# Kernel optimization log

Measured on AMD Instinct MI355X. Metric: run time of the kernel, lower is better.

## Reference

```python
import jax, jax.numpy as jnp
import numpy as np

N_NODES = 100000
N_EDGES = 3200000
B = 64            # number of graphs / RNA batch
DIM = 16          # GINE hidden dim
NFP = 33          # protein node feature dim
EMB = 128         # embedding dim
MAXLEN = 3000     # rna_global length (conv1d in_channels)
LOCLEN = 2998     # rna_local length = 3000 - log4(64) + 1
NF = 32           # n_filters
KS = 8            # conv kernel size -> 128-8+1 = 121
FC_IN = NF * 121  # 3872
BN_EPS = 1e-5


def setup_inputs() -> dict:
    key = jax.random.key(0)
    ks = jax.random.split(key, 32)
    s = 0.1
    p = {}
    # forward data args
    p['pro_x'] = jax.random.normal(ks[0], (N_NODES, NFP), jnp.float32)
    p['pro_edge_index'] = jax.random.randint(ks[1], (2, N_EDGES), 0, N_NODES, jnp.int32)
    p['pro_weight'] = jax.random.uniform(ks[2], (N_EDGES, 1), jnp.float32)
    p['pro_batch'] = jnp.sort(jax.random.randint(ks[3], (N_NODES,), 0, B, jnp.int32))
    p['rna_global'] = jax.random.randint(ks[4], (B, MAXLEN), 0, 5, jnp.int32)
    p['rna_local'] = jax.random.randint(ks[5], (B, LOCLEN), 0, 65, jnp.int32)
    # GINE layer 1 (33 -> 16)
    p['g1_w1'] = jax.random.normal(ks[6], (NFP, DIM), jnp.float32) * s
    p['g1_b1'] = jnp.zeros((DIM,), jnp.float32)
    p['g1_w2'] = jax.random.normal(ks[7], (DIM, DIM), jnp.float32) * s
    p['g1_b2'] = jnp.zeros((DIM,), jnp.float32)
    p['g1_ew'] = jax.random.normal(ks[8], (1, NFP), jnp.float32) * s  # edge Linear(1, 33)
    p['g1_eb'] = jnp.zeros((NFP,), jnp.float32)
    p['g1_eps'] = jnp.zeros((), jnp.float32)
    # GINE layers 2-5 (16 -> 16), stacked on leading axis
    p['g_w1'] = jax.random.normal(ks[9], (4, DIM, DIM), jnp.float32) * s
    p['g_b1'] = jnp.zeros((4, DIM), jnp.float32)
    p['g_w2'] = jax.random.normal(ks[10], (4, DIM, DIM), jnp.float32) * s
    p['g_b2'] = jnp.zeros((4, DIM), jnp.float32)
    p['g_ew'] = jax.random.normal(ks[11], (4, 1, DIM), jnp.float32) * s  # edge Linear(1, 16)
    p['g_eb'] = jnp.zeros((4, DIM), jnp.float32)
    p['g_eps'] = jnp.zeros((4,), jnp.float32)
    # BatchNorm1d x5
    p['bn_gamma'] = jnp.ones((5, DIM), jnp.float32)
    p['bn_beta'] = jnp.zeros((5, DIM), jnp.float32)
    # fc1_xp (16 -> 128)
    p['fc1_xp_w'] = jax.random.normal(ks[12], (DIM, EMB), jnp.float32) * s
    p['fc1_xp_b'] = jnp.zeros((EMB,), jnp.float32)
    # RNA branch
    p['emb1'] = jax.random.normal(ks[13], (5, EMB), jnp.float32)
    p['emb2'] = jax.random.normal(ks[14], (65, EMB), jnp.float32)
    p['convr1_w'] = jax.random.normal(ks[15], (NF, MAXLEN, KS), jnp.float32) * 0.01
    p['convr1_b'] = jnp.zeros((NF,), jnp.float32)
    p['convr2_w'] = jax.random.normal(ks[16], (NF, LOCLEN, KS), jnp.float32) * 0.01
    p['convr2_b'] = jnp.zeros((NF,), jnp.float32)
    p['fcxr_w'] = jax.random.normal(ks[17], (FC_IN, EMB), jnp.float32) * 0.01
    p['fcxr_b'] = jnp.zeros((EMB,), jnp.float32)
    return p


def _gine(x, src, dst, ew, w1, b1, w2, b2, ew_w, ew_b, eps):
    # GINEConv: out = MLP((1+eps)*x + sum_j relu(x_j + edge_lin(e_ij)))
    e = ew @ ew_w + ew_b                       # [E, d]
    m = jax.nn.relu(x[src] + e)                # [E, d] gather + fuse
    agg = jax.ops.segment_sum(m, dst, num_segments=N_NODES)
    h = (1.0 + eps) * x + agg
    return jax.nn.relu(h @ w1 + b1) @ w2 + b2


def _bn(x, gamma, beta):
    mu = jnp.mean(x, axis=0)
    var = jnp.var(x, axis=0)
    return (x - mu) * jax.lax.rsqrt(var + BN_EPS) * gamma + beta


def _rna_branch(tokens, emb, cw, cb, fcw, fcb):
    x = emb[tokens]                            # [B, L, 128]
    y = jax.lax.conv_general_dilated(x, cw, (1,), 'VALID',
                                     dimension_numbers=('NCH', 'OIH', 'NCH'))
    y = y + cb[None, :, None]                  # [B, 32, 121]
    return y.reshape(y.shape[0], -1) @ fcw + fcb


def reference(pro_x, pro_edge_index, pro_weight, pro_batch, rna_global, rna_local,
              g1_w1, g1_b1, g1_w2, g1_b2, g1_ew, g1_eb, g1_eps,
              g_w1, g_b1, g_w2, g_b2, g_ew, g_eb, g_eps,
              bn_gamma, bn_beta, fc1_xp_w, fc1_xp_b,
              emb1, emb2, convr1_w, convr1_b, convr2_w, convr2_b, fcxr_w, fcxr_b):
    src, dst = pro_edge_index[0], pro_edge_index[1]
    # RNA global / local branches (shared fc_xr)
    xrg = _rna_branch(rna_global, emb1, convr1_w, convr1_b, fcxr_w, fcxr_b)
    xrl = _rna_branch(rna_local, emb2, convr2_w, convr2_b, fcxr_w, fcxr_b)
    # protein GINE stack
    xp = jax.nn.relu(_gine(pro_x, src, dst, pro_weight,
                           g1_w1, g1_b1, g1_w2, g1_b2, g1_ew, g1_eb, g1_eps))
    xp = _bn(xp, bn_gamma[0], bn_beta[0])
    for i in range(4):
        xp = jax.nn.relu(_gine(xp, src, dst, pro_weight,
                               g_w1[i], g_b1[i], g_w2[i], g_b2[i],
                               g_ew[i], g_eb[i], g_eps[i]))
        xp = _bn(xp, bn_gamma[i + 1], bn_beta[i + 1])
    # global mean pool over graphs
    sums = jax.ops.segment_sum(xp, pro_batch, num_segments=B)
    cnt = jax.ops.segment_sum(jnp.ones((N_NODES, 1), xp.dtype), pro_batch, num_segments=B)
    xp = jax.nn.relu((sums / jnp.maximum(cnt, 1.0)) @ fc1_xp_w + fc1_xp_b)
    # dropout in eval mode -> identity
    xc_rna = 0.5 * (xrg + xrl)
    return (xc_rna, xp)
```

## Files before the change

kernel.cpp:

```cpp
#include <hip/hip_runtime.h>
#include <hip/hip_fp16.h>

#define N_NODES 100000
#define N_EDGES 3200000
#define BGR 64
#define DIM 16
#define NFP 33
#define ROW1 32
#define H1STR 36
#define EMB 128
#define MAXLEN 3000
#define LOCLEN 2998
#define NF 32
#define KS 8
#define OUTT 121
#define FC_IN 3872
#define BN_EPSV 1e-5f
#define POOL_CHUNK 256
#define POOL_BLKS 391
#define MLPB 391
#define AGGB1 6250
#define AGGB16 3125
#define NBIN 391
#define BCNT_BLK 512
#define P1_CHUNK 4096
#define P1_BLOCKS 782
#define MAXBIN 9088
#define NKC 32
#define KCH 121
#define WDEC (1.f / 32767.f)
#define SEG_G 8

__global__ void __launch_bounds__(256) k_bincnt(const int* __restrict__ dst,
                                                int* __restrict__ bh) {
    __shared__ int hist[NBIN];
    int t = threadIdx.x, bid = blockIdx.x;
    for (int b = t; b < NBIN; b += 256) hist[b] = 0;
    __syncthreads();
    int e0 = bid * (N_EDGES / BCNT_BLK);
    int e1 = e0 + (N_EDGES / BCNT_BLK);
    for (int e = e0 + t; e < e1; e += 256) atomicAdd(&hist[dst[e] >> 8], 1);
    __syncthreads();
    for (int b = t; b < NBIN; b += 256) bh[b * BCNT_BLK + bid] = hist[b];
}

__global__ void __launch_bounds__(512) k_binscan(const int* __restrict__ bh,
                                                 int* __restrict__ binoff,
                                                 int* __restrict__ bincur) {
    __shared__ int sc[512];
    int t = threadIdx.x;
    int s = 0;
    if (t < NBIN) {
        const int4* row = (const int4*)(bh + t * BCNT_BLK);
        #pragma unroll 4
        for (int k = 0; k < BCNT_BLK / 4; k++) {
            int4 v = row[k];
            s += v.x + v.y + v.z + v.w;
        }
    }
    sc[t] = s;
    __syncthreads();
    for (int off = 1; off < 512; off <<= 1) {
        int v = (t >= off) ? sc[t - off] : 0;
        __syncthreads();
        sc[t] += v;
        __syncthreads();
    }
    int excl = sc[t] - s;
    if (t <= NBIN) binoff[t] = excl;
    if (t < NBIN) bincur[t] = excl;
}

__global__ void __launch_bounds__(256) k_part1(const int* __restrict__ src,
                                               const int* __restrict__ dst,
                                               const float* __restrict__ w,
                                               int* __restrict__ bincur,
                                               int2* __restrict__ tmp_sw) {
    __shared__ int2 srec[P1_CHUNK];
    __shared__ unsigned short sbin[P1_CHUNK];
    __shared__ unsigned short sperm[P1_CHUNK];
    __shared__ int hist[NBIN];
    __shared__ int off[NBIN];
    __shared__ int cur[NBIN];
    __shared__ int base[NBIN];
    __shared__ int sc[512];
    int t = threadIdx.x;
    int g0 = blockIdx.x * P1_CHUNK;
    int cn = N_EDGES - g0; if (cn > P1_CHUNK) cn = P1_CHUNK;
    for (int b = t; b < NBIN; b += 256) hist[b] = 0;
    __syncthreads();
    for (int j = t; j < cn; j += 256) {
        int d = dst[g0 + j];
        int b = d >> 8;
        sbin[j] = (unsigned short)b;
        srec[j] = make_int2(src[g0 + j] | ((d & 255) << 20), __float_as_int(w[g0 + j]));
        atomicAdd(&hist[b], 1);
    }
    __syncthreads();
    sc[t] = (t < NBIN) ? hist[t] : 0;
    sc[256 + t] = (256 + t < NBIN) ? hist[256 + t] : 0;
    __syncthreads();
    for (int o = 1; o <= 256; o <<= 1) {
        int v0 = (t >= o) ? sc[t - o] : 0;
        int v1 = sc[256 + t - o];
        __syncthreads();
        sc[t] += v0;
        sc[256 + t] += v1;
        __syncthreads();
    }
    for (int b = t; b < NBIN; b += 256) {
        int e = sc[b] - hist[b];
        off[b] = e;
        cur[b] = e;
        int c = hist[b];
        base[b] = c ? atomicAdd(&bincur[b], c) : 0;
    }
    __syncthreads();
    for (int j = t; j < cn; j += 256) {
        int p = atomicAdd(&cur[sbin[j]], 1);
        sperm[p] = (unsigned short)j;
    }
    __syncthreads();
    for (int p = t; p < cn; p += 256) {
        int j = sperm[p];
        int b = sbin[j];
        tmp_sw[base[b] + (p - off[b])] = srec[j];
    }
}

__global__ void __launch_bounds__(256) k_part2(const int2* __restrict__ tmp_sw,
                                               const int* __restrict__ binoff,
                                               unsigned* __restrict__ er,
                                               int* __restrict__ ptr) {
    __shared__ unsigned char sdl[MAXBIN];
    __shared__ unsigned short perm[MAXBIN];
    __shared__ int hist[256];
    __shared__ int cur[256];
    __shared__ int sc[256];
    int t = threadIdx.x, b = blockIdx.x;
    int nlo = b << 8;
    int e0 = binoff[b], e1 = binoff[b + 1];
    int cnt = e1 - e0;
    int stage = cnt < MAXBIN ? cnt : MAXBIN;
    hist[t] = 0;
    __syncthreads();
    for (int j = t; j < stage; j += 256) {
        unsigned char dl = (unsigned char)((tmp_sw[e0 + j].x >> 20) & 255);
        sdl[j] = dl;
        atomicAdd(&hist[dl], 1);
    }
    for (int j = stage + t; j < cnt; j += 256)
        atomicAdd(&hist[(tmp_sw[e0 + j].x >> 20) & 255], 1);
    __syncthreads();
    int v = hist[t];
    sc[t] = v;
    __syncthreads();
    for (int off = 1; off < 256; off <<= 1) {
        int u = (t >= off) ? sc[t - off] : 0;
        __syncthreads();
        sc[t] += u;
        __syncthreads();
    }
    int excl = sc[t] - v;
    cur[t] = excl;
    if (nlo + t < N_NODES) ptr[nlo + t] = e0 + excl;
    if (b == NBIN - 1 && t == 0) ptr[N_NODES] = N_EDGES;
    __syncthreads();
    for (int j = t; j < stage; j += 256) {
        int p = atomicAdd(&cur[sdl[j]], 1);
        perm[p] = (unsigned short)j;
    }
    __syncthreads();
    for (int j = stage + t; j < cnt; j += 256) {
        int2 sw = tmp_sw[e0 + j];
        int p = atomicAdd(&cur[(sw.x >> 20) & 255], 1);
        unsigned wq = (unsigned)(__int_as_float(sw.y) * 32767.f + 0.5f);
        er[e0 + p] = ((unsigned)sw.x & 0x1FFFFu) | (wq << 17);
    }
    for (int p = t; p < stage; p += 256) {
        int2 sw = tmp_sw[e0 + perm[p]];
        unsigned wq = (unsigned)(__int_as_float(sw.y) * 32767.f + 0.5f);
        er[e0 + p] = ((unsigned)sw.x & 0x1FFFFu) | (wq << 17);
    }
}

__global__ void k_half1(const float* __restrict__ x, __half* __restrict__ xh,
                        __half* __restrict__ xh32) {
    int i = blockIdx.x * blockDim.x + threadIdx.x;
    if (i < N_NODES * NFP) {
        int n = i / NFP, f = i - n * NFP;
        __half v = __float2half(x[i]);
        if (f < 32) xh[n * ROW1 + f] = v;
        else xh32[n] = v;
    }
}

__global__ void __launch_bounds__(256) k_cwt2(const float* __restrict__ cw1,
                                              const float* __restrict__ cw2,
                                              float* __restrict__ cwTg,
                                              float* __restrict__ cwTl) {
    int l = blockIdx.x;
    int ok = threadIdx.x;
    if (l < MAXLEN) {
        cwTg[l * 256 + ok] = cw1[(ok >> 3) * (MAXLEN * KS) + l * KS + (ok & 7)];
    } else {
        int ll = l - MAXLEN;
        cwTl[ll * 256 + ok] = cw2[(ok >> 3) * (LOCLEN * KS) + ll * KS + (ok & 7)];
    }
}

__device__ __forceinline__ void acc8p(float a[8], uint4 r, float wv,
                                      const float* __restrict__ ewf,
                                      const float* __restrict__ ebf) {
    float2 f01 = __half22float2(*(__half2*)&r.x);
    float2 f23 = __half22float2(*(__half2*)&r.y);
    float2 f45 = __half22float2(*(__half2*)&r.z);
    float2 f67 = __half22float2(*(__half2*)&r.w);
    float x[8] = {f01.x, f01.y, f23.x, f23.y, f45.x, f45.y, f67.x, f67.y};
    #pragma unroll
    for (int j = 0; j < 8; j++)
        a[j] += fmaxf(x[j] + fmaf(wv, ewf[j], ebf[j]), 0.f);
}

__device__ __forceinline__ void acc8s(float a[8], uint4 r, float wv,
                                      const float* __restrict__ scf,
                                      const float* __restrict__ cbf,
                                      const float* __restrict__ ewf) {
    float2 f01 = __half22float2(*(__half2*)&r.x);
    float2 f23 = __half22float2(*(__half2*)&r.y);
    float2 f45 = __half22float2(*(__half2*)&r.z);
    float2 f67 = __half22float2(*(__half2*)&r.w);
    float x[8] = {f01.x, f01.y, f23.x, f23.y, f45.x, f45.y, f67.x, f67.y};
    #pragma unroll
    for (int j = 0; j < 8; j++)
        a[j] += fmaxf(fmaf(x[j], scf[j], fmaf(wv, ewf[j], cbf[j])), 0.f);
}

__global__ void __launch_bounds__(256) k_agg1(
    const __half* __restrict__ xh, const __half* __restrict__ xh32,
    const int* __restrict__ ptr, const unsigned* __restrict__ er,
    const float* __restrict__ ew, const float* __restrict__ ebv,
    const float* __restrict__ epsp, float* __restrict__ h) {
    int t = threadIdx.x;
    int wave = t >> 6, lane = t & 63;
    int nl = lane >> 4;
    int slot = (lane >> 2) & 3;
    int q = lane & 3;
    float ewf[8], ebf[8];
    #pragma unroll
    for (int j = 0; j < 8; j++) { ewf[j] = ew[q * 8 + j]; ebf[j] = ebv[q * 8 + j]; }
    float ew32 = ew[32], eb32 = ebv[32];
    float ep = 1.f + epsp[0];
    int node = blockIdx.x * 16 + wave * 4 + nl;
    int e0 = ptr[node], e1 = ptr[node + 1];
    float a[8] = {0, 0, 0, 0, 0, 0, 0, 0};
    float a32 = 0.f;
    int i = e0 + slot;
    while (i + 4 < e1) {
        unsigned ev0 = er[i];
        unsigned ev1 = er[i + 4];
        int s0 = ev0 & 0x1FFFF, s1 = ev1 & 0x1FFFF;
        float wv0 = (float)(ev0 >> 17) * WDEC;
        float wv1 = (float)(ev1 >> 17) * WDEC;
        uint4 r0 = *(const uint4*)(xh + s0 * ROW1 + q * 8);
        uint4 r1 = *(const uint4*)(xh + s1 * ROW1 + q * 8);
        acc8p(a, r0, wv0, ewf, ebf);
        acc8p(a, r1, wv1, ewf, ebf);
        if (q == 0) {
            a32 += fmaxf(__half2float(xh32[s0]) + fmaf(wv0, ew32, eb32), 0.f);
            a32 += fmaxf(__half2float(xh32[s1]) + fmaf(wv1, ew32, eb32), 0.f);
        }
        i += 8;
    }
    if (i < e1) {
        unsigned ev = er[i];
        int s = ev & 0x1FFFF;
        float wv = (float)(ev >> 17) * WDEC;
        uint4 r = *(const uint4*)(xh + s * ROW1 + q * 8);
        acc8p(a, r, wv, ewf, ebf);
        if (q == 0)
            a32 += fmaxf(__half2float(xh32[s]) + fmaf(wv, ew32, eb32), 0.f);
    }
    #pragma unroll
    for (int j = 0; j < 8; j++) {
        a[j] += __shfl_xor(a[j], 4);
        a[j] += __shfl_xor(a[j], 8);
    }
    a32 += __shfl_xor(a32, 4);
    a32 += __shfl_xor(a32, 8);
    if (slot == 0) {
        uint4 sraw = *(const uint4*)(xh + node * ROW1 + q * 8);
        float2 s01 = __half22float2(*(__half2*)&sraw.x);
        float2 s23 = __half22float2(*(__half2*)&sraw.y);
        float2 s45 = __half22float2(*(__half2*)&sraw.z);
        float2 s67 = __half22float2(*(__half2*)&sraw.w);
        float* hp = h + node * H1STR + q * 8;
        *(float4*)hp = make_float4(ep * s01.x + a[0], ep * s01.y + a[1],
                                   ep * s23.x + a[2], ep * s23.y + a[3]);
        *(float4*)(hp + 4) = make_float4(ep * s45.x + a[4], ep * s45.y + a[5],
                                         ep * s67.x + a[6], ep * s67.y + a[7]);
        if (q == 0)
            h[node * H1STR + 32] = ep * __half2float(xh32[node]) + a32;
    }
}

__global__ void __launch_bounds__(256) k_agg16(
    const __half* __restrict__ zh, const int* __restrict__ ptr,
    const unsigned* __restrict__ er,
    const float* __restrict__ ew, const float* __restrict__ ebv,
    const float* __restrict__ epsp,
    const float* __restrict__ bnstat, const float* __restrict__ gamma,
    const float* __restrict__ beta, float* __restrict__ h) {
    int t = threadIdx.x;
    int wave = t >> 6, lane = t & 63;
    int nl = lane >> 3;
    int slot = (lane >> 1) & 3;
    int hh = lane & 1;
    float ep = 1.f + epsp[0];
    const float invn = 1.f / (float)N_NODES;
    float scf[8], shf[8], cbf[8], ewf[8];
    #pragma unroll
    for (int j = 0; j < 8; j++) {
        int f = hh * 8 + j;
        float mu = bnstat[f] * invn;
        float var = bnstat[DIM + f] * invn - mu * mu;
        float sc = gamma[f] * rsqrtf(var + BN_EPSV);
        scf[j] = sc;
        shf[j] = beta[f] - mu * sc;
        cbf[j] = shf[j] + ebv[f];
        ewf[j] = ew[f];
    }
    int node = blockIdx.x * 32 + wave * 8 + nl;
    int e0 = ptr[node], e1 = ptr[node + 1];
    float a[8] = {0, 0, 0, 0, 0, 0, 0, 0};
    int i = e0 + slot;
    while (i + 4 < e1) {
        unsigned ev0 = er[i];
        unsigned ev1 = er[i + 4];
        float wv0 = (float)(ev0 >> 17) * WDEC;
        float wv1 = (float)(ev1 >> 17) * WDEC;
        uint4 r0 = *(const uint4*)(zh + (ev0 & 0x1FFFFu) * DIM + hh * 8);
        uint4 r1 = *(const uint4*)(zh + (ev1 & 0x1FFFFu) * DIM + hh * 8);
        acc8s(a, r0, wv0, scf, cbf, ewf);
        acc8s(a, r1, wv1, scf, cbf, ewf);
        i += 8;
    }
    if (i < e1) {
        unsigned ev = er[i];
        float wv = (float)(ev >> 17) * WDEC;
        uint4 r = *(const uint4*)(zh + (ev & 0x1FFFFu) * DIM + hh * 8);
        acc8s(a, r, wv, scf, cbf, ewf);
    }
    #pragma unroll
    for (int j = 0; j < 8; j++) a[j] += __shfl_xor(a[j], 2);
    #pragma unroll
    for (int j = 0; j < 8; j++) a[j] += __shfl_xor(a[j], 4);
    if (slot == 0) {
        uint4 sraw = *(const uint4*)(zh + node * DIM + hh * 8);
        float2 s01 = __half22float2(*(__half2*)&sraw.x);
        float2 s23 = __half22float2(*(__half2*)&sraw.y);
        float2 s45 = __half22float2(*(__half2*)&sraw.z);
        float2 s67 = __half22float2(*(__half2*)&sraw.w);
        float xs[8] = {s01.x, s01.y, s23.x, s23.y, s45.x, s45.y, s67.x, s67.y};
        float o8[8];
        #pragma unroll
        for (int j = 0; j < 8; j++)
            o8[j] = ep * fmaf(xs[j], scf[j], shf[j]) + a[j];
        float* hp = h + node * DIM + hh * 8;
        *(float4*)hp = make_float4(o8[0], o8[1], o8[2], o8[3]);
        *(float4*)(hp + 4) = make_float4(o8[4], o8[5], o8[6], o8[7]);
    }
}

__device__ __forceinline__ void mlp_bn_tail(float zv[16], bool active, int t,
                                            float* __restrict__ bnstat) {
    __shared__ float red[4][32];
    float zs[16], zq[16];
    #pragma unroll
    for (int o = 0; o < 16; o++) {
        zs[o] = active ? zv[o] : 0.f;
        zq[o] = active ? zv[o] * zv[o] : 0.f;
    }
    #pragma unroll
    for (int m = 1; m <= 32; m <<= 1) {
        #pragma unroll
        for (int o = 0; o < 16; o++) {
            zs[o] += __shfl_xor(zs[o], m);
            zq[o] += __shfl_xor(zq[o], m);
        }
    }
    int wave = t >> 6, lane = t & 63;
    if (lane == 0) {
        #pragma unroll
        for (int o = 0; o < 16; o++) {
            red[wave][o] = zs[o];
            red[wave][16 + o] = zq[o];
        }
    }
    __syncthreads();
    if (t < 32)
        atomicAdd(&bnstat[t], red[0][t] + red[1][t] + red[2][t] + red[3][t]);
}

__device__ __forceinline__ void store_zh(__half* __restrict__ zh, int n, float zv[16]) {
    __half2 p[8];
    #pragma unroll
    for (int j = 0; j < 8; j++) p[j] = __floats2half2_rn(zv[2 * j], zv[2 * j + 1]);
    *(uint4*)(zh + n * DIM) = *(uint4*)&p[0];
    *(uint4*)(zh + n * DIM + 8) = *(uint4*)&p[4];
}

__global__ void __launch_bounds__(256) k_mlp16(
    const float* __restrict__ h,
    const float* __restrict__ W1, const float* __restrict__ b1,
    const float* __restrict__ W2, const float* __restrict__ b2,
    __half* __restrict__ zh, float* __restrict__ bnstat) {
    __shared__ float W1s[256], W2s[256], b1s[16], b2s[16];
    int t = threadIdx.x;
    W1s[t] = W1[t];
    W2s[t] = W2[t];
    if (t < 16) { b1s[t] = b1[t]; b2s[t] = b2[t]; }
    __syncthreads();
    int n = blockIdx.x * 256 + t;
    bool active = n < N_NODES;
    float zv[16];
    if (active) {
        float hv[16];
        #pragma unroll
        for (int j = 0; j < 4; j++) {
            float4 v = *(const float4*)(h + n * DIM + j * 4);
            hv[j * 4] = v.x; hv[j * 4 + 1] = v.y; hv[j * 4 + 2] = v.z; hv[j * 4 + 3] = v.w;
        }
        float tv[16];
        #pragma unroll
        for (int o = 0; o < 16; o++) {
            float s = b1s[o];
            #pragma unroll
            for (int f = 0; f < 16; f++) s += hv[f] * W1s[f * 16 + o];
            tv[o] = fmaxf(s, 0.f);
        }
        #pragma unroll
        for (int o = 0; o < 16; o++) {
            float s = b2s[o];
            #pragma unroll
            for (int f = 0; f < 16; f++) s += tv[f] * W2s[f * 16 + o];
            zv[o] = fmaxf(s, 0.f);
        }
        store_zh(zh, n, zv);
    }
    mlp_bn_tail(zv, active, t, bnstat);
}

__global__ void __launch_bounds__(256) k_mlp1(
    const float* __restrict__ h,
    const float* __restrict__ W1, const float* __restrict__ b1,
    const float* __restrict__ W2, const float* __restrict__ b2,
    __half* __restrict__ zh, float* __restrict__ bnstat) {
    __shared__ float W1s[NFP * 16], W2s[256], b1s[16], b2s[16];
    int t = threadIdx.x;
    for (int j = t; j < NFP * 16; j += 256) W1s[j] = W1[j];
    W2s[t] = W2[t];
    if (t < 16) { b1s[t] = b1[t]; b2s[t] = b2[t]; }
    __syncthreads();
    int n = blockIdx.x * 256 + t;
    bool active = n < N_NODES;
    float zv[16];
    if (active) {
        float hv[NFP];
        #pragma unroll
        for (int j = 0; j < 8; j++) {
            float4 v = *(const float4*)(h + n * H1STR + j * 4);
            hv[j * 4] = v.x; hv[j * 4 + 1] = v.y; hv[j * 4 + 2] = v.z; hv[j * 4 + 3] = v.w;
        }
        hv[32] = h[n * H1STR + 32];
        float tv[16];
        #pragma unroll
        for (int o = 0; o < 16; o++) {
            float s = b1s[o];
            #pragma unroll
            for (int f = 0; f < NFP; f++) s += hv[f] * W1s[f * 16 + o];
            tv[o] = fmaxf(s, 0.f);
        }
        #pragma unroll
        for (int o = 0; o < 16; o++) {
            float s = b2s[o];
            #pragma unroll
            for (int f = 0; f < 16; f++) s += tv[f] * W2s[f * 16 + o];
            zv[o] = fmaxf(s, 0.f);
        }
        store_zh(zh, n, zv);
    }
    mlp_bn_tail(zv, active, t, bnstat);
}

__global__ void __launch_bounds__(256) k_pool(const __half* __restrict__ zh,
                                              const int* __restrict__ batch,
                                              const float* __restrict__ bnstat,
                                              const float* __restrict__ gamma,
                                              const float* __restrict__ beta,
                                              float* __restrict__ gsum,
                                              float* __restrict__ gcnt) {
    __shared__ float lsum[BGR * DIM];
    __shared__ float lcnt[BGR];
    int t = threadIdx.x;
    for (int j = t; j < BGR * DIM; j += 256) lsum[j] = 0.f;
    if (t < BGR) lcnt[t] = 0.f;
    __syncthreads();
    int f = t & 15, r = t >> 4;
    const float invn = 1.f / (float)N_NODES;
    float mu = bnstat[f] * invn;
    float var = bnstat[DIM + f] * invn - mu * mu;
    float sc = gamma[f] * rsqrtf(var + BN_EPSV);
    float sh = beta[f] - mu * sc;
    int start = blockIdx.x * POOL_CHUNK;
    float acc = 0.f, cacc = 0.f;
    int cur = -1;
    for (int i = 0; i < POOL_CHUNK / 16; i++) {
        int n = start + r + i * 16;
        if (n >= N_NODES) break;
        int b = batch[n];
        if (b != cur) {
            if (cur >= 0) {
                atomicAdd(&lsum[cur * DIM + f], acc);
                if (f == 0) atomicAdd(&lcnt[cur], cacc);
            }
            cur = b; acc = 0.f; cacc = 0.f;
        }
        acc += fmaf(__half2float(zh[n * DIM + f]), sc, sh);
        cacc += 1.f;
    }
    if (cur >= 0) {
        atomicAdd(&lsum[cur * DIM + f], acc);
        if (f == 0) atomicAdd(&lcnt[cur], cacc);
    }
    __syncthreads();
    for (int j = t; j < BGR * DIM; j += 256) {
        float v = lsum[j];
        if (v != 0.f) atomicAdd(&gsum[j], v);
    }
    if (t < BGR) {
        float v = lcnt[t];
        if (v != 0.f) atomicAdd(&gcnt[t], v);
    }
}

__global__ void k_xp(const float* __restrict__ gsum, const float* __restrict__ gcnt,
                     const float* __restrict__ w, const float* __restrict__ bias,
                     float* __restrict__ out) {
    int b = blockIdx.x;
    int e = threadIdx.x;
    float inv = 1.f / fmaxf(gcnt[b], 1.f);
    float acc = bias[e];
    #pragma unroll
    for (int f = 0; f < DIM; f++) acc += gsum[b * DIM + f] * inv * w[f * EMB + e];
    out[b * EMB + e] = fmaxf(acc, 0.f);
}

__global__ void __launch_bounds__(256) k_bucket2(const int* __restrict__ tg,
                                                 const int* __restrict__ tl,
                                                 int* __restrict__ blg, int* __restrict__ bpg,
                                                 int* __restrict__ bll, int* __restrict__ bpl) {
    __shared__ int hist[65];
    __shared__ int cursor[65];
    int which = blockIdx.y;
    const int* tok = which ? tl : tg;
    int L = which ? LOCLEN : MAXLEN;
    int V = which ? 65 : 5;
    int* blist = which ? bll : blg;
    int* bptr = which ? bpl : bpg;
    int b = blockIdx.x, t = threadIdx.x;
    if (t < V) hist[t] = 0;
    __syncthreads();
    for (int l = t; l < L; l += 256) atomicAdd(&hist[tok[b * L + l]], 1);
    __syncthreads();
    if (t == 0) {
        int run = 0;
        for (int v = 0; v < V; v++) {
            cursor[v] = run;
            bptr[b * (V + 1) + v] = run;
            run += hist[v];
        }
        bptr[b * (V + 1) + V] = run;
    }
    __syncthreads();
    for (int l = t; l < L; l += 256) {
        int v = tok[b * L + l];
        int p = atomicAdd(&cursor[v], 1);
        blist[b * L + p] = l;
    }
}

__global__ void __launch_bounds__(256) k_wsum(const int* __restrict__ blg,
                                              const int* __restrict__ bpg,
                                              const int* __restrict__ bll,
                                              const int* __restrict__ bpl,
                                              const float* __restrict__ cwTg,
                                              const float* __restrict__ cwTl,
                                              float* __restrict__ Wp,
                                              float* __restrict__ Wlocal) {
    int b = blockIdx.x, y = blockIdx.y;
    int t = threadIdx.x;
    if (y < 40) {
        int v = y >> 3, seg = y & 7;
        int s = bpg[b * 6 + v], e = bpg[b * 6 + v + 1];
        int cnt = e - s;
        int chunk = (cnt + SEG_G - 1) / SEG_G;
        int j0 = s + seg * chunk;
        int j1 = j0 + chunk; if (j1 > e) j1 = e;
        const int* bl = blg + b * MAXLEN;
        float acc = 0.f;
        int j = j0;
        while (j + 3 < j1) {
            int t0 = bl[j], t1 = bl[j + 1], t2 = bl[j + 2], t3 = bl[j + 3];
            float a0 = cwTg[t0 * 256 + t];
            float a1 = cwTg[t1 * 256 + t];
            float a2 = cwTg[t2 * 256 + t];
            float a3 = cwTg[t3 * 256 + t];
            acc += a0 + a1 + a2 + a3;
            j += 4;
        }
        while (j < j1) {
            acc += cwTg[bl[j] * 256 + t];
            j++;
        }
        Wp[((b * 5 + v) * SEG_G + seg) * 256 + t] = acc;
    } else {
        int v = y - 40;
        int s = bpl[b * 66 + v], e = bpl[b * 66 + v + 1];
        const int* bl = bll + b * LOCLEN;
        float acc = 0.f;
        int j = s;
        while (j + 3 < e) {
            int t0 = bl[j], t1 = bl[j + 1], t2 = bl[j + 2], t3 = bl[j + 3];
            float a0 = cwTl[t0 * 256 + t];
            float a1 = cwTl[t1 * 256 + t];
            float a2 = cwTl[t2 * 256 + t];
            float a3 = cwTl[t3 * 256 + t];
            acc += a0 + a1 + a2 + a3;
            j += 4;
        }
        while (j < e) {
            acc += cwTl[bl[j] * 256 + t];
            j++;
        }
        int o = t >> 3, k = t & 7;
        Wlocal[((b * NF + o) * 65 + v) * KS + k] = acc;
    }
}

__global__ void __launch_bounds__(128) k_yfc(const float* __restrict__ Wpg,
                                             const float* __restrict__ Wl,
                                             const float* __restrict__ emb1,
                                             const float* __restrict__ emb2,
                                             const float* __restrict__ cb1,
                                             const float* __restrict__ cb2,
                                             const float* __restrict__ w,
                                             float* __restrict__ partial) {
    int which = blockIdx.y;
    int bo = blockIdx.x;
    int b = bo >> 5, o = bo & 31;
    int t = threadIdx.x;
    const float* emb = which ? emb2 : emb1;
    const float* cb = which ? cb2 : cb1;
    int V = which ? 65 : 5;
    __shared__ float Wsh[65 * KS];
    __shared__ float ych[OUTT];
    if (which) {
        const float* Wrow = Wl + (b * NF + o) * 65 * KS;
        for (int j = t; j < 65 * KS; j += 128) Wsh[j] = Wrow[j];
    } else {
        for (int j = t; j < 5 * KS; j += 128) {
            int v = j >> 3, k = j & 7;
            const float* p = Wpg + (b * 5 + v) * SEG_G * 256 + o * 8 + k;
            float s = 0.f;
            #pragma unroll
            for (int g = 0; g < SEG_G; g++) s += p[g * 256];
            Wsh[j] = s;
        }
    }
    __syncthreads();
    if (t < OUTT) {
        float acc = cb[o];
        for (int v = 0; v < V; v++) {
            const float* ep = emb + v * EMB + t;
            #pragma unroll
            for (int k = 0; k < KS; k++) acc += Wsh[v * KS + k] * ep[k];
        }
        ych[t] = acc;
    }
    __syncthreads();
    float facc = 0.f;
    const float* wp = w + (o * OUTT) * EMB + t;
    #pragma unroll 4
    for (int jj = 0; jj < OUTT; jj++) facc += ych[jj] * wp[jj * EMB];
    partial[((which * BGR + b) * NKC + o) * EMB + t] = facc;
}

__global__ void k_fcred(const float* __restrict__ partial, const float* __restrict__ bias,
                        float* __restrict__ out) {
    int b = blockIdx.x;
    int e = threadIdx.x;
    const float* pg = partial + b * NKC * EMB + e;
    const float* pl = partial + (BGR + b) * NKC * EMB + e;
    float ag = bias[e], al = bias[e];
    #pragma unroll
    for (int k = 0; k < NKC; k++) { ag += pg[k * EMB]; al += pl[k * EMB]; }
    out[b * EMB + e] = 0.5f * (ag + al);
}

extern "C" void kernel_launch(void* const* d_in, const int* in_sizes, int n_in,
                              void* d_out, int out_size, void* d_ws, size_t ws_size,
                              hipStream_t stream) {
    const float* pro_x = (const float*)d_in[0];
    const int* eidx = (const int*)d_in[1];
    const int* esrc = eidx;
    const int* edst = eidx + N_EDGES;
    const float* pw = (const float*)d_in[2];
    const int* batch = (const int*)d_in[3];
    const int* rg = (const int*)d_in[4];
    const int* rl = (const int*)d_in[5];
    const float* g1_w1 = (const float*)d_in[6];
    const float* g1_b1 = (const float*)d_in[7];
    const float* g1_w2 = (const float*)d_in[8];
    const float* g1_b2 = (const float*)d_in[9];
    const float* g1_ew = (const float*)d_in[10];
    const float* g1_eb = (const float*)d_in[11];
    const float* g1_eps = (const float*)d_in[12];
    const float* g_w1 = (const float*)d_in[13];
    const float* g_b1 = (const float*)d_in[14];
    const float* g_w2 = (const float*)d_in[15];
    const float* g_b2 = (const float*)d_in[16];
    const float* g_ew = (const float*)d_in[17];
    const float* g_eb = (const float*)d_in[18];
    const float* g_eps = (const float*)d_in[19];
    const float* bn_gamma = (const float*)d_in[20];
    const float* bn_beta = (const float*)d_in[21];
    const float* fc1_xp_w = (const float*)d_in[22];
    const float* fc1_xp_b = (const float*)d_in[23];
    const float* emb1 = (const float*)d_in[24];
    const float* emb2 = (const float*)d_in[25];
    const float* convr1_w = (const float*)d_in[26];
    const float* convr1_b = (const float*)d_in[27];
    const float* convr2_w = (const float*)d_in[28];
    const float* convr2_b = (const float*)d_in[29];
    const float* fcxr_w = (const float*)d_in[30];
    const float* fcxr_b = (const float*)d_in[31];
    float* out = (float*)d_out;

    float* wsf = (float*)d_ws;
    int* ptr       = (int*)wsf;        wsf += 100128;
    int* binoff    = (int*)wsf;        wsf += 512;
    int* bincur    = (int*)wsf;        wsf += 512;
    unsigned* er   = (unsigned*)wsf;   wsf += 2 * N_EDGES;
    float* stats   = wsf;              wsf += 1280;
    float* un = wsf;
    int2* tmp_sw = (int2*)un;
    int* bh      = (int*)(un + 7200000);
    float* cwTg  = un;
    float* cwTl  = un + 768000;
    __half* zh   = (__half*)(un + 1600000);
    __half* xh1  = (__half*)(un + 2400000);
    __half* xh32 = (__half*)(un + 4000000);
    float* Wpg   = un + 4300000;
    float* Wl    = un + 5000000;
    int* blg     = (int*)(un + 6600000);
    int* bll     = (int*)(un + 6800000);
    int* bpg     = (int*)(un + 7000000);
    int* bpl     = (int*)(un + 7001000);
    float* fcpart = un + 7100000;
    float* h      = un + 7400000;
    float* gsum   = stats;
    float* gcnt   = stats + 1024;
    float* bnstat = stats + 1088;

    hipMemsetAsync(stats, 0, 1280 * sizeof(float), stream);

    k_bincnt<<<BCNT_BLK, 256, 0, stream>>>(edst, bh);
    k_binscan<<<1, 512, 0, stream>>>(bh, binoff, bincur);
    k_part1<<<P1_BLOCKS, 256, 0, stream>>>(esrc, edst, pw, bincur, tmp_sw);
    k_part2<<<NBIN, 256, 0, stream>>>(tmp_sw, binoff, er, ptr);

    k_cwt2<<<MAXLEN + LOCLEN, 256, 0, stream>>>(convr1_w, convr2_w, cwTg, cwTl);

    k_half1<<<(N_NODES * NFP + 255) / 256, 256, 0, stream>>>(pro_x, xh1, xh32);

    k_bucket2<<<dim3(BGR, 2), 256, 0, stream>>>(rg, rl, blg, bpg, bll, bpl);
    k_wsum<<<dim3(BGR, 105), 256, 0, stream>>>(blg, bpg, bll, bpl, cwTg, cwTl, Wpg, Wl);
    k_yfc<<<dim3(BGR * NF, 2), 128, 0, stream>>>(Wpg, Wl, emb1, emb2, convr1_b, convr2_b,
                                                 fcxr_w, fcpart);
    k_fcred<<<BGR, 128, 0, stream>>>(fcpart, fcxr_b, out);

    k_agg1<<<AGGB1, 256, 0, stream>>>(xh1, xh32, ptr, er, g1_ew, g1_eb, g1_eps, h);
    k_mlp1<<<MLPB, 256, 0, stream>>>(h, g1_w1, g1_b1, g1_w2, g1_b2, zh, bnstat);
    for (int i = 0; i < 4; i++) {
        k_agg16<<<AGGB16, 256, 0, stream>>>(zh, ptr, er,
                                            g_ew + i * DIM, g_eb + i * DIM, g_eps + i,
                                            bnstat + i * 32, bn_gamma + i * DIM,
                                            bn_beta + i * DIM, h);
        k_mlp16<<<MLPB, 256, 0, stream>>>(h, g_w1 + i * DIM * DIM, g_b1 + i * DIM,
                                          g_w2 + i * DIM * DIM, g_b2 + i * DIM, zh,
                                          bnstat + (i + 1) * 32);
    }
    k_pool<<<POOL_BLKS, 256, 0, stream>>>(zh, batch, bnstat + 4 * 32,
                                          bn_gamma + 4 * DIM, bn_beta + 4 * DIM, gsum, gcnt);
    k_xp<<<BGR, EMB, 0, stream>>>(gsum, gcnt, fc1_xp_w, fc1_xp_b, out + BGR * EMB);
}
```

Before: 571.5 us.

## Fuse GINE aggregation with MLP and BN stats, merge small preprocessing kernels

Fuses the 16-dim edge aggregation with the two-layer MLP and the BatchNorm statistics reduction into one kernel per layer. It ping-pongs fp16 node buffers so no layer reads the buffer it writes. This removes the fp32 intermediate h round-trip and one launch per layer. The preprocessing kernels (bin count with RNA bucketing, conv-weight transpose with fp16 conversion) and the final FC reductions are also merged to cut launch count. In exchange, every lane of the node group now does the MLP redundantly, and the fused kernel adds shared-memory weight loads, syncthreads and more register pressure.

```diff
diff --git a/kernel.cpp b/kernel.cpp
--- a/kernel.cpp
+++ b/kernel.cpp
@@ -31,17 +31,52 @@
 #define WDEC (1.f / 32767.f)
 #define SEG_G 8
 
-__global__ void __launch_bounds__(256) k_bincnt(const int* __restrict__ dst,
-                                                int* __restrict__ bh) {
-    __shared__ int hist[NBIN];
+__global__ void __launch_bounds__(256) k_pre1(const int* __restrict__ dst,
+                                              int* __restrict__ bh,
+                                              const int* __restrict__ rg,
+                                              const int* __restrict__ rl,
+                                              int* __restrict__ blg, int* __restrict__ bpg,
+                                              int* __restrict__ bll, int* __restrict__ bpl) {
+    __shared__ int sh[NBIN];
     int t = threadIdx.x, bid = blockIdx.x;
-    for (int b = t; b < NBIN; b += 256) hist[b] = 0;
-    __syncthreads();
-    int e0 = bid * (N_EDGES / BCNT_BLK);
-    int e1 = e0 + (N_EDGES / BCNT_BLK);
-    for (int e = e0 + t; e < e1; e += 256) atomicAdd(&hist[dst[e] >> 8], 1);
-    __syncthreads();
-    for (int b = t; b < NBIN; b += 256) bh[b * BCNT_BLK + bid] = hist[b];
+    if (bid < BCNT_BLK) {
+        for (int b = t; b < NBIN; b += 256) sh[b] = 0;
+        __syncthreads();
+        int e0 = bid * (N_EDGES / BCNT_BLK);
+        int e1 = e0 + (N_EDGES / BCNT_BLK);
+        for (int e = e0 + t; e < e1; e += 256) atomicAdd(&sh[dst[e] >> 8], 1);
+        __syncthreads();
+        for (int b = t; b < NBIN; b += 256) bh[b * BCNT_BLK + bid] = sh[b];
+    } else {
+        int idx = bid - BCNT_BLK;
+        int which = idx >> 6, b = idx & 63;
+        const int* tok = which ? rl : rg;
+        int L = which ? LOCLEN : MAXLEN;
+        int V = which ? 65 : 5;
+        int* blist = which ? bll : blg;
+        int* bptr = which ? bpl : bpg;
+        int* hist = sh;
+        int* cursor = sh + 70;
+        if (t < V) hist[t] = 0;
+        __syncthreads();
+        for (int l = t; l < L; l += 256) atomicAdd(&hist[tok[b * L + l]], 1);
+        __syncthreads();
+        if (t == 0) {
+            int run = 0;
+            for (int v = 0; v < V; v++) {
+                cursor[v] = run;
+                bptr[b * (V + 1) + v] = run;
+                run += hist[v];
+            }
+            bptr[b * (V + 1) + V] = run;
+        }
+        __syncthreads();
+        for (int l = t; l < L; l += 256) {
+            int v = tok[b * L + l];
+            int p = atomicAdd(&cursor[v], 1);
+            blist[b * L + p] = l;
+        }
+    }
 }
 
 __global__ void __launch_bounds__(512) k_binscan(const int* __restrict__ bh,
@@ -184,28 +219,27 @@
     }
 }
 
-__global__ void k_half1(const float* __restrict__ x, __half* __restrict__ xh,
-                        __half* __restrict__ xh32) {
-    int i = blockIdx.x * blockDim.x + threadIdx.x;
-    if (i < N_NODES * NFP) {
-        int n = i / NFP, f = i - n * NFP;
-        __half v = __float2half(x[i]);
-        if (f < 32) xh[n * ROW1 + f] = v;
-        else xh32[n] = v;
-    }
-}
-
-__global__ void __launch_bounds__(256) k_cwt2(const float* __restrict__ cw1,
+__global__ void __launch_bounds__(256) k_pre2(const float* __restrict__ cw1,
                                               const float* __restrict__ cw2,
                                               float* __restrict__ cwTg,
-                                              float* __restrict__ cwTl) {
-    int l = blockIdx.x;
-    int ok = threadIdx.x;
-    if (l < MAXLEN) {
-        cwTg[l * 256 + ok] = cw1[(ok >> 3) * (MAXLEN * KS) + l * KS + (ok & 7)];
+                                              float* __restrict__ cwTl,
+                                              const float* __restrict__ x,
+                                              __half* __restrict__ xh,
+                                              __half* __restrict__ xh32) {
+    int bid = blockIdx.x, t = threadIdx.x;
+    if (bid < MAXLEN) {
+        cwTg[bid * 256 + t] = cw1[(t >> 3) * (MAXLEN * KS) + bid * KS + (t & 7)];
+    } else if (bid < MAXLEN + LOCLEN) {
+        int ll = bid - MAXLEN;
+        cwTl[ll * 256 + t] = cw2[(t >> 3) * (LOCLEN * KS) + ll * KS + (t & 7)];
     } else {
-        int ll = l - MAXLEN;
-        cwTl[ll * 256 + ok] = cw2[(ok >> 3) * (LOCLEN * KS) + ll * KS + (ok & 7)];
+        int i = (bid - (MAXLEN + LOCLEN)) * 256 + t;
+        if (i < N_NODES * NFP) {
+            int n = i / NFP, f = i - n * NFP;
+            __half v = __float2half(x[i]);
+            if (f < 32) xh[n * ROW1 + f] = v;
+            else xh32[n] = v;
+        }
     }
 }
 
@@ -304,14 +338,23 @@
     }
 }
 
-__global__ void __launch_bounds__(256) k_agg16(
-    const __half* __restrict__ zh, const int* __restrict__ ptr,
+__global__ void __launch_bounds__(256) k_f16(
+    const __half* __restrict__ zin, const int* __restrict__ ptr,
     const unsigned* __restrict__ er,
     const float* __restrict__ ew, const float* __restrict__ ebv,
     const float* __restrict__ epsp,
     const float* __restrict__ bnstat, const float* __restrict__ gamma,
-    const float* __restrict__ beta, float* __restrict__ h) {
+    const float* __restrict__ beta,
+    const float* __restrict__ W1, const float* __restrict__ b1,
+    const float* __restrict__ W2, const float* __restrict__ b2,
+    __half* __restrict__ zout, float* __restrict__ bnout) {
+    __shared__ float W1s[256], W2s[256], b1s[16], b2s[16];
+    __shared__ float red[4][32];
     int t = threadIdx.x;
+    W1s[t] = W1[t];
+    W2s[t] = W2[t];
+    if (t < 16) { b1s[t] = b1[t]; b2s[t] = b2[t]; }
+    __syncthreads();
     int wave = t >> 6, lane = t & 63;
     int nl = lane >> 3;
     int slot = (lane >> 1) & 3;
@@ -339,8 +382,8 @@
         unsigned ev1 = er[i + 4];
         float wv0 = (float)(ev0 >> 17) * WDEC;
         float wv1 = (float)(ev1 >> 17) * WDEC;
-        uint4 r0 = *(const uint4*)(zh + (ev0 & 0x1FFFFu) * DIM + hh * 8);
-        uint4 r1 = *(const uint4*)(zh + (ev1 & 0x1FFFFu) * DIM + hh * 8);
+        uint4 r0 = *(const uint4*)(zin + (ev0 & 0x1FFFFu) * DIM + hh * 8);
+        uint4 r1 = *(const uint4*)(zin + (ev1 & 0x1FFFFu) * DIM + hh * 8);
         acc8s(a, r0, wv0, scf, cbf, ewf);
         acc8s(a, r1, wv1, scf, cbf, ewf);
         i += 8;
@@ -348,28 +391,93 @@
     if (i < e1) {
         unsigned ev = er[i];
         float wv = (float)(ev >> 17) * WDEC;
-        uint4 r = *(const uint4*)(zh + (ev & 0x1FFFFu) * DIM + hh * 8);
+        uint4 r = *(const uint4*)(zin + (ev & 0x1FFFFu) * DIM + hh * 8);
         acc8s(a, r, wv, scf, cbf, ewf);
     }
     #pragma unroll
     for (int j = 0; j < 8; j++) a[j] += __shfl_xor(a[j], 2);
     #pragma unroll
     for (int j = 0; j < 8; j++) a[j] += __shfl_xor(a[j], 4);
+    uint4 sraw = *(const uint4*)(zin + node * DIM + hh * 8);
+    float2 s01 = __half22float2(*(__half2*)&sraw.x);
+    float2 s23 = __half22float2(*(__half2*)&sraw.y);
+    float2 s45 = __half22float2(*(__half2*)&sraw.z);
+    float2 s67 = __half22float2(*(__half2*)&sraw.w);
+    float xs[8] = {s01.x, s01.y, s23.x, s23.y, s45.x, s45.y, s67.x, s67.y};
+    float o8[8];
+    #pragma unroll
+    for (int j = 0; j < 8; j++)
+        o8[j] = ep * fmaf(xs[j], scf[j], shf[j]) + a[j];
+    float oth[8];
+    #pragma unroll
+    for (int j = 0; j < 8; j++) oth[j] = __shfl_xor(o8[j], 1);
+    float hv[16];
+    if (hh == 0) {
+        #pragma unroll
+        for (int j = 0; j < 8; j++) { hv[j] = o8[j]; hv[8 + j] = oth[j]; }
+    } else {
+        #pragma unroll
+        for (int j = 0; j < 8; j++) { hv[j] = oth[j]; hv[8 + j] = o8[j]; }
+    }
+    int ob = hh * 8;
+    float tv[8];
+    #pragma unroll
+    for (int j = 0; j < 8; j++) {
+        float s = b1s[ob + j];
+        #pragma unroll
+        for (int f = 0; f < 16; f++) s += hv[f] * W1s[f * 16 + ob + j];
+        tv[j] = fmaxf(s, 0.f);
+    }
+    float tvo[8];
+    #pragma unroll
+    for (int j = 0; j < 8; j++) tvo[j] = __shfl_xor(tv[j], 1);
+    float tf[16];
+    if (hh == 0) {
+        #pragma unroll
+        for (int j = 0; j < 8; j++) { tf[j] = tv[j]; tf[8 + j] = tvo[j]; }
+    } else {
+        #pragma unroll
+        for (int j = 0; j < 8; j++) { tf[j] = tvo[j]; tf[8 + j] = tv[j]; }
+    }
+    float zv[8];
+    #pragma unroll
+    for (int j = 0; j < 8; j++) {
+        float s = b2s[ob + j];
+        #pragma unroll
+        for (int f = 0; f < 16; f++) s += tf[f] * W2s[f * 16 + ob + j];
+        zv[j] = fmaxf(s, 0.f);
+    }
     if (slot == 0) {
-        uint4 sraw = *(const uint4*)(zh + node * DIM + hh * 8);
-        float2 s01 = __half22float2(*(__half2*)&sraw.x);
-        float2 s23 = __half22float2(*(__half2*)&sraw.y);
-        float2 s45 = __half22float2(*(__half2*)&sraw.z);
-        float2 s67 = __half22float2(*(__half2*)&sraw.w);
-        float xs[8] = {s01.x, s01.y, s23.x, s23.y, s45.x, s45.y, s67.x, s67.y};
-        float o8[8];
-        #pragma unroll
-        for (int j = 0; j < 8; j++)
-            o8[j] = ep * fmaf(xs[j], scf[j], shf[j]) + a[j];
-        float* hp = h + node * DIM + hh * 8;
-        *(float4*)hp = make_float4(o8[0], o8[1], o8[2], o8[3]);
-        *(float4*)(hp + 4) = make_float4(o8[4], o8[5], o8[6], o8[7]);
-    }
+        __half2 p[4];
+        #pragma unroll
+        for (int j = 0; j < 4; j++) p[j] = __floats2half2_rn(zv[2 * j], zv[2 * j + 1]);
+        *(uint4*)(zout + node * DIM + hh * 8) = *(uint4*)&p[0];
+    }
+    float zs[8], zq[8];
+    bool act = (slot == 0);
+    #pragma unroll
+    for (int j = 0; j < 8; j++) {
+        zs[j] = act ? zv[j] : 0.f;
+        zq[j] = act ? zv[j] * zv[j] : 0.f;
+    }
+    #pragma unroll
+    for (int m = 8; m <= 32; m <<= 1) {
+        #pragma unroll
+        for (int j = 0; j < 8; j++) {
+            zs[j] += __shfl_xor(zs[j], m);
+            zq[j] += __shfl_xor(zq[j], m);
+        }
+    }
+    if (lane < 2) {
+        #pragma unroll
+        for (int j = 0; j < 8; j++) {
+            red[wave][lane * 8 + j] = zs[j];
+            red[wave][16 + lane * 8 + j] = zq[j];
+        }
+    }
+    __syncthreads();
+    if (t < 32)
+        atomicAdd(&bnout[t], red[0][t] + red[1][t] + red[2][t] + red[3][t]);
 }
 
 __device__ __forceinline__ void mlp_bn_tail(float zv[16], bool active, int t,
@@ -408,47 +516,6 @@
     for (int j = 0; j < 8; j++) p[j] = __floats2half2_rn(zv[2 * j], zv[2 * j + 1]);
     *(uint4*)(zh + n * DIM) = *(uint4*)&p[0];
     *(uint4*)(zh + n * DIM + 8) = *(uint4*)&p[4];
-}
-
-__global__ void __launch_bounds__(256) k_mlp16(
-    const float* __restrict__ h,
-    const float* __restrict__ W1, const float* __restrict__ b1,
-    const float* __restrict__ W2, const float* __restrict__ b2,
-    __half* __restrict__ zh, float* __restrict__ bnstat) {
-    __shared__ float W1s[256], W2s[256], b1s[16], b2s[16];
-    int t = threadIdx.x;
-    W1s[t] = W1[t];
-    W2s[t] = W2[t];
-    if (t < 16) { b1s[t] = b1[t]; b2s[t] = b2[t]; }
-    __syncthreads();
-    int n = blockIdx.x * 256 + t;
-    bool active = n < N_NODES;
-    float zv[16];
-    if (active) {
-        float hv[16];
-        #pragma unroll
-        for (int j = 0; j < 4; j++) {
-            float4 v = *(const float4*)(h + n * DIM + j * 4);
-            hv[j * 4] = v.x; hv[j * 4 + 1] = v.y; hv[j * 4 + 2] = v.z; hv[j * 4 + 3] = v.w;
-        }
-        float tv[16];
-        #pragma unroll
-        for (int o = 0; o < 16; o++) {
-            float s = b1s[o];
-            #pragma unroll
-            for (int f = 0; f < 16; f++) s += hv[f] * W1s[f * 16 + o];
-            tv[o] = fmaxf(s, 0.f);
-        }
-        #pragma unroll
-        for (int o = 0; o < 16; o++) {
-            float s = b2s[o];
-            #pragma unroll
-            for (int f = 0; f < 16; f++) s += tv[f] * W2s[f * 16 + o];
-            zv[o] = fmaxf(s, 0.f);
-        }
-        store_zh(zh, n, zv);
-    }
-    mlp_bn_tail(zv, active, t, bnstat);
 }
 
 __global__ void __launch_bounds__(256) k_mlp1(
@@ -541,52 +608,6 @@
     if (t < BGR) {
         float v = lcnt[t];
         if (v != 0.f) atomicAdd(&gcnt[t], v);
-    }
-}
-
-__global__ void k_xp(const float* __restrict__ gsum, const float* __restrict__ gcnt,
-                     const float* __restrict__ w, const float* __restrict__ bias,
-                     float* __restrict__ out) {
-    int b = blockIdx.x;
-    int e = threadIdx.x;
-    float inv = 1.f / fmaxf(gcnt[b], 1.f);
-    float acc = bias[e];
-    #pragma unroll
-    for (int f = 0; f < DIM; f++) acc += gsum[b * DIM + f] * inv * w[f * EMB + e];
-    out[b * EMB + e] = fmaxf(acc, 0.f);
-}
-
-__global__ void __launch_bounds__(256) k_bucket2(const int* __restrict__ tg,
-                                                 const int* __restrict__ tl,
-                                                 int* __restrict__ blg, int* __restrict__ bpg,
-                                                 int* __restrict__ bll, int* __restrict__ bpl) {
-    __shared__ int hist[65];
-    __shared__ int cursor[65];
-    int which = blockIdx.y;
-    const int* tok = which ? tl : tg;
-    int L = which ? LOCLEN : MAXLEN;
-    int V = which ? 65 : 5;
-    int* blist = which ? bll : blg;
-    int* bptr = which ? bpl : bpg;
-    int b = blockIdx.x, t = threadIdx.x;
-    if (t < V) hist[t] = 0;
-    __syncthreads();
-    for (int l = t; l < L; l += 256) atomicAdd(&hist[tok[b * L + l]], 1);
-    __syncthreads();
-    if (t == 0) {
-        int run = 0;
-        for (int v = 0; v < V; v++) {
-            cursor[v] = run;
-            bptr[b * (V + 1) + v] = run;
-            run += hist[v];
-        }
-        bptr[b * (V + 1) + V] = run;
-    }
-    __syncthreads();
-    for (int l = t; l < L; l += 256) {
-        int v = tok[b * L + l];
-        int p = atomicAdd(&cursor[v], 1);
-        blist[b * L + p] = l;
     }
 }
 
@@ -696,16 +717,29 @@
     partial[((which * BGR + b) * NKC + o) * EMB + t] = facc;
 }
 
-__global__ void k_fcred(const float* __restrict__ partial, const float* __restrict__ bias,
-                        float* __restrict__ out) {
+__global__ void __launch_bounds__(128) k_tail(const float* __restrict__ partial,
+                                              const float* __restrict__ bias,
+                                              const float* __restrict__ gsum,
+                                              const float* __restrict__ gcnt,
+                                              const float* __restrict__ w,
+                                              const float* __restrict__ xpb,
+                                              float* __restrict__ out) {
     int b = blockIdx.x;
     int e = threadIdx.x;
-    const float* pg = partial + b * NKC * EMB + e;
-    const float* pl = partial + (BGR + b) * NKC * EMB + e;
-    float ag = bias[e], al = bias[e];
-    #pragma unroll
-    for (int k = 0; k < NKC; k++) { ag += pg[k * EMB]; al += pl[k * EMB]; }
-    out[b * EMB + e] = 0.5f * (ag + al);
+    if (blockIdx.y == 0) {
+        const float* pg = partial + b * NKC * EMB + e;
+        const float* pl = partial + (BGR + b) * NKC * EMB + e;
+        float ag = bias[e], al = bias[e];
+        #pragma unroll
+        for (int k = 0; k < NKC; k++) { ag += pg[k * EMB]; al += pl[k * EMB]; }
+        out[b * EMB + e] = 0.5f * (ag + al);
+    } else {
+        float inv = 1.f / fmaxf(gcnt[b], 1.f);
+        float acc = xpb[e];
+        #pragma unroll
+        for (int f = 0; f < DIM; f++) acc += gsum[b * DIM + f] * inv * w[f * EMB + e];
+        out[BGR * EMB + b * EMB + e] = fmaxf(acc, 0.f);
+    }
 }
 
 extern "C" void kernel_launch(void* const* d_in, const int* in_sizes, int n_in,
@@ -758,7 +792,7 @@
     int* bh      = (int*)(un + 7200000);
     float* cwTg  = un;
     float* cwTl  = un + 768000;
-    __half* zh   = (__half*)(un + 1600000);
+    __half* zhA  = (__half*)(un + 1600000);
     __half* xh1  = (__half*)(un + 2400000);
     __half* xh32 = (__half*)(un + 4000000);
     float* Wpg   = un + 4300000;
@@ -767,41 +801,43 @@
     int* bll     = (int*)(un + 6800000);
     int* bpg     = (int*)(un + 7000000);
     int* bpl     = (int*)(un + 7001000);
-    float* fcpart = un + 7100000;
+    float* fcpart = un + 6600000;
     float* h      = un + 7400000;
+    __half* zhB  = (__half*)(un + 10200000);
     float* gsum   = stats;
     float* gcnt   = stats + 1024;
     float* bnstat = stats + 1088;
 
     hipMemsetAsync(stats, 0, 1280 * sizeof(float), stream);
 
-    k_bincnt<<<BCNT_BLK, 256, 0, stream>>>(edst, bh);
+    k_pre1<<<BCNT_BLK + 128, 256, 0, stream>>>(edst, bh, rg, rl, blg, bpg, bll, bpl);
     k_binscan<<<1, 512, 0, stream>>>(bh, binoff, bincur);
     k_part1<<<P1_BLOCKS, 256, 0, stream>>>(esrc, edst, pw, bincur, tmp_sw);
     k_part2<<<NBIN, 256, 0, stream>>>(tmp_sw, binoff, er, ptr);
 
-    k_cwt2<<<MAXLEN + LOCLEN, 256, 0, stream>>>(convr1_w, convr2_w, cwTg, cwTl);
-
-    k_half1<<<(N_NODES * NFP + 255) / 256, 256, 0, stream>>>(pro_x, xh1, xh32);
-
-    k_bucket2<<<dim3(BGR, 2), 256, 0, stream>>>(rg, rl, blg, bpg, bll, bpl);
+    k_pre2<<<MAXLEN + LOCLEN + (N_NODES * NFP + 255) / 256, 256, 0, stream>>>(
+        convr1_w, convr2_w, cwTg, cwTl, pro_x, xh1, xh32);
+
     k_wsum<<<dim3(BGR, 105), 256, 0, stream>>>(blg, bpg, bll, bpl, cwTg, cwTl, Wpg, Wl);
     k_yfc<<<dim3(BGR * NF, 2), 128, 0, stream>>>(Wpg, Wl, emb1, emb2, convr1_b, convr2_b,
                                                  fcxr_w, fcpart);
-    k_fcred<<<BGR, 128, 0, stream>>>(fcpart, fcxr_b, out);
 
     k_agg1<<<AGGB1, 256, 0, stream>>>(xh1, xh32, ptr, er, g1_ew, g1_eb, g1_eps, h);
-    k_mlp1<<<MLPB, 256, 0, stream>>>(h, g1_w1, g1_b1, g1_w2, g1_b2, zh, bnstat);
-    for (int i = 0; i < 4; i++) {
-        k_agg16<<<AGGB16, 256, 0, stream>>>(zh, ptr, er,
-                                            g_ew + i * DIM, g_eb + i * DIM, g_eps + i,
-                                            bnstat + i * 32, bn_gamma + i * DIM,
-                                            bn_beta + i * DIM, h);
-        k_mlp16<<<MLPB, 256, 0, stream>>>(h, g_w1 + i * DIM * DIM, g_b1 + i * DIM,
-                                          g_w2 + i * DIM * DIM, g_b2 + i * DIM, zh,
-                                          bnstat + (i + 1) * 32);
-    }
-    k_pool<<<POOL_BLKS, 256, 0, stream>>>(zh, batch, bnstat + 4 * 32,
+    k_mlp1<<<MLPB, 256, 0, stream>>>(h, g1_w1, g1_b1, g1_w2, g1_b2, zhA, bnstat);
+    {
+        __half* zi[5] = {zhA, zhB, zhA, zhB, zhA};
+        for (int i = 0; i < 4; i++) {
+            k_f16<<<AGGB16, 256, 0, stream>>>(zi[i], ptr, er,
+                                              g_ew + i * DIM, g_eb + i * DIM, g_eps + i,
+                                              bnstat + i * 32, bn_gamma + i * DIM,
+                                              bn_beta + i * DIM,
+                                              g_w1 + i * DIM * DIM, g_b1 + i * DIM,
+                                              g_w2 + i * DIM * DIM, g_b2 + i * DIM,
+                                              zi[i + 1], bnstat + (i + 1) * 32);
+        }
+    }
+    k_pool<<<POOL_BLKS, 256, 0, stream>>>(zhA, batch, bnstat + 4 * 32,
                                           bn_gamma + 4 * DIM, bn_beta + 4 * DIM, gsum, gcnt);
-    k_xp<<<BGR, EMB, 0, stream>>>(gsum, gcnt, fc1_xp_w, fc1_xp_b, out + BGR * EMB);
-}
+    k_tail<<<dim3(BGR, 2), 128, 0, stream>>>(fcpart, fcxr_b, gsum, gcnt,
+                                             fc1_xp_w, fc1_xp_b, out);
+}
```

Result: slower. 647.4 us (+13.3%).
